# Performance work log

Hardware: AMD Instinct MI355X
Metric: run time of the kernel (lower is better)

## Reference

```python
import jax, jax.numpy as jnp
import numpy as np
from jax.ops import segment_sum

N_NODES = 50000
N_EDGES = 800000
N_GRAPHS = 64
N_CLASSES = 100
HEADS = 5
EPS = 1e-5


def _self_loops(edge_index, n):
    loop = jnp.arange(n, dtype=edge_index.dtype)
    src = jnp.concatenate([edge_index[0], loop])
    dst = jnp.concatenate([edge_index[1], loop])
    return src, dst


def gcn_conv(x, src, dst, n, w, b):
    xw = x @ w  # [N, C]
    deg = segment_sum(jnp.ones_like(dst, dtype=xw.dtype), dst, num_segments=n)
    dis = jnp.where(deg > 0, jax.lax.rsqrt(jnp.maximum(deg, 1.0)), 0.0)
    norm = dis[src] * dis[dst]  # [E']
    out = segment_sum(norm[:, None] * xw[src], dst, num_segments=n)
    return out + b


def batch_norm(x, gamma, beta):
    mu = jnp.mean(x, axis=0)
    var = jnp.var(x, axis=0)
    return (x - mu) * jax.lax.rsqrt(var + EPS) * gamma + beta


def gcn_block(x, src, dst, n, w, b, gamma, beta, residual):
    h = jax.nn.gelu(batch_norm(gcn_conv(x, src, dst, n, w, b), gamma, beta), approximate=False)
    return h + x if residual else h


def gat_conv(x, src, dst, n, w, att_src, att_dst, bias):
    H, C = att_src.shape
    xw = (x @ w).reshape(n, H, C)  # [N,H,C]
    a_src = jnp.sum(xw * att_src, axis=-1)  # [N,H]
    a_dst = jnp.sum(xw * att_dst, axis=-1)  # [N,H]
    e = jax.nn.leaky_relu(a_src[src] + a_dst[dst], 0.2)  # [E',H]
    m = jax.ops.segment_max(e, dst, num_segments=n)
    alpha = jnp.exp(e - m[dst])
    denom = segment_sum(alpha, dst, num_segments=n)
    alpha = alpha / jnp.maximum(denom[dst], 1e-16)
    # loop over small fixed head count to bound memory of [E',C] gathers
    outs = []
    for h in range(H):
        msg = alpha[:, h:h + 1] * xw[src, h, :]  # [E',C]
        outs.append(segment_sum(msg, dst, num_segments=n))
    out = jnp.mean(jnp.stack(outs, axis=0), axis=0)  # concat=False -> mean over heads
    return out + bias


def graph_layer_norm(x, gamma, beta):
    # PyG LayerNorm(mode='graph') with batch=None: normalize over all nodes+features
    mu = jnp.mean(x)
    var = jnp.var(x)
    return (x - mu) * jax.lax.rsqrt(var + EPS) * gamma + beta


def layer_norm(x, gamma, beta):
    mu = jnp.mean(x, axis=-1, keepdims=True)
    var = jnp.var(x, axis=-1, keepdims=True)
    return (x - mu) * jax.lax.rsqrt(var + EPS) * gamma + beta


def global_mean_pool(x, batch, n_graphs):
    sums = segment_sum(x, batch, num_segments=n_graphs)
    cnt = segment_sum(jnp.ones((x.shape[0],), x.dtype), batch, num_segments=n_graphs)
    return sums / jnp.maximum(cnt, 1.0)[:, None]


def setup_inputs() -> dict:
    key = jax.random.key(0)
    ks = jax.random.split(key, 24)
    glorot = lambda k, shp: jax.random.normal(k, shp, jnp.float32) * np.sqrt(2.0 / (shp[0] + shp[-1]))
    inp = {}
    inp['x'] = jax.random.normal(ks[0], (N_NODES, 3), jnp.float32)
    inp['edge_index'] = jax.random.randint(ks[1], (2, N_EDGES), 0, N_NODES, jnp.int64)
    inp['batch'] = jnp.sort(jax.random.randint(ks[2], (N_NODES,), 0, N_GRAPHS, jnp.int64))
    # input block 3->128
    inp['w_in'] = glorot(ks[3], (3, 128)); inp['b_in'] = jnp.zeros((128,), jnp.float32)
    inp['g_in'] = jnp.ones((128,), jnp.float32); inp['be_in'] = jnp.zeros((128,), jnp.float32)
    # hidden block 128->128 (n_hidden_blocks=2 -> one hidden block)
    inp['w_h'] = glorot(ks[4], (128, 128)); inp['b_h'] = jnp.zeros((128,), jnp.float32)
    inp['g_h'] = jnp.ones((128,), jnp.float32); inp['be_h'] = jnp.zeros((128,), jnp.float32)
    # GAT 128 -> 5 heads x 128, mean
    inp['w_gat'] = glorot(ks[5], (128, HEADS * 128))
    inp['att_src'] = glorot(ks[6], (HEADS, 128)); inp['att_dst'] = glorot(ks[7], (HEADS, 128))
    inp['b_gat'] = jnp.zeros((128,), jnp.float32)
    # output block 128->512
    inp['w_out'] = glorot(ks[8], (128, 512)); inp['b_out'] = jnp.zeros((512,), jnp.float32)
    inp['g_out'] = jnp.ones((512,), jnp.float32); inp['be_out'] = jnp.zeros((512,), jnp.float32)
    # encoder layer norm
    inp['g_ln'] = jnp.ones((512,), jnp.float32); inp['be_ln'] = jnp.zeros((512,), jnp.float32)
    # projection head
    inp['w_p1'] = glorot(ks[9], (512, 128)); inp['b_p1'] = jnp.zeros((128,), jnp.float32)
    inp['g_pbn'] = jnp.ones((128,), jnp.float32); inp['be_pbn'] = jnp.zeros((128,), jnp.float32)
    inp['w_p2'] = glorot(ks[10], (128, 128)); inp['b_p2'] = jnp.zeros((128,), jnp.float32)
    inp['g_pln'] = jnp.ones((128,), jnp.float32); inp['be_pln'] = jnp.zeros((128,), jnp.float32)
    # classifier
    inp['w_c'] = glorot(ks[11], (128, N_CLASSES)); inp['b_c'] = jnp.zeros((N_CLASSES,), jnp.float32)
    return inp


def reference(x, edge_index, batch, w_in, b_in, g_in, be_in, w_h, b_h, g_h, be_h,
              w_gat, att_src, att_dst, b_gat, w_out, b_out, g_out, be_out,
              g_ln, be_ln, w_p1, b_p1, g_pbn, be_pbn, w_p2, b_p2, g_pln, be_pln,
              w_c, b_c):
    n = x.shape[0]
    src, dst = _self_loops(edge_index, n)
    # encoder
    h = gcn_block(x, src, dst, n, w_in, b_in, g_in, be_in, residual=False)
    h = gcn_block(h, src, dst, n, w_h, b_h, g_h, be_h, residual=True)
    h = gat_conv(h, src, dst, n, w_gat, att_src, att_dst, b_gat)
    h = gcn_block(h, src, dst, n, w_out, b_out, g_out, be_out, residual=False)
    h = graph_layer_norm(h, g_ln, be_ln)
    h = global_mean_pool(h, batch, N_GRAPHS)  # [G,512]
    # projection head
    p = jax.nn.gelu(batch_norm(h @ w_p1 + b_p1, g_pbn, be_pbn), approximate=False)
    p = layer_norm(p @ w_p2 + b_p2 + p, g_pln, be_pln)
    # normalize + classifier
    x1 = p / jnp.maximum(jnp.linalg.norm(p, axis=1, keepdims=True), 1e-12)
    c1 = jax.nn.log_softmax(x1 @ w_c + b_c, axis=1)
    return (x1, c1)
```

## Files before the change

### kernel.cpp

```cpp
#include <hip/hip_runtime.h>
#include <hip/hip_bf16.h>
#include <math.h>

#define NN 50000
#define NE 800000
#define NG 64
#define NC 100
#define EPSV 1e-5f
#define PBN 256
#define SCB 196
#define SPL 8
#define PRB 128

typedef unsigned int   u32;
typedef unsigned short u16;
typedef __attribute__((ext_vector_type(8))) short bf16x8;
typedef __attribute__((ext_vector_type(4))) float f32x4;

__device__ __forceinline__ float gelu_f(float x){
  return 0.5f*x*(1.0f + erff(x*0.70710678118654752f));
}
__device__ __forceinline__ float bf2f(u16 u){
  return __uint_as_float(((u32)u)<<16);
}
__device__ __forceinline__ float2 bf2f2(u32 u){
  float2 r;
  r.x = __uint_as_float(u<<16);
  r.y = __uint_as_float(u & 0xffff0000u);
  return r;
}
__device__ __forceinline__ u16 f2bf(float f){
  __hip_bfloat16 h = __float2bfloat16(f);
  return *(u16*)&h;
}
__device__ __forceinline__ u32 pack_bf2(float a, float b){
  return (u32)f2bf(a) | ((u32)f2bf(b)<<16);
}

__global__ void k_deg_init(int* deg){
  int i = blockIdx.x*256 + threadIdx.x;
  if (i < NN) deg[i] = 1;
}
__global__ void k_deg_hist(const int* ei, int* deg){
  int e = blockIdx.x*256 + threadIdx.x;
  if (e < NE) atomicAdd(&deg[ei[NE + e]], 1);
}
__global__ void k_scanA(const int* deg, int* bsum, float* dis){
  __shared__ int red[256];
  int b = blockIdx.x, t = threadIdx.x;
  int i = b*256 + t;
  int d = (i < NN) ? deg[i] : 1;
  if (i < NN) dis[i] = rsqrtf((float)d);
  red[t] = (i < NN) ? d-1 : 0;
  __syncthreads();
  for (int st = 128; st; st >>= 1){
    if (t < st) red[t] += red[t+st];
    __syncthreads();
  }
  if (t == 0) bsum[b] = red[0];
}
__global__ void k_scanB(const int* bsum, int* boff){
  __shared__ int sh[256];
  int t = threadIdx.x;
  sh[t] = (t < SCB) ? bsum[t] : 0;
  __syncthreads();
  for (int d = 1; d < 256; d <<= 1){
    int v = (t >= d) ? sh[t-d] : 0;
    __syncthreads();
    sh[t] += v;
    __syncthreads();
  }
  if (t == 0) boff[0] = 0;
  if (t < SCB) boff[t+1] = sh[t];
}
__global__ void k_scanC(const int* deg, const int* boff, int* off, int* cur){
  __shared__ int sh[256];
  int b = blockIdx.x, t = threadIdx.x;
  int i = b*256 + t;
  int v = (i < NN) ? deg[i]-1 : 0;
  sh[t] = v;
  __syncthreads();
  for (int d = 1; d < 256; d <<= 1){
    int u = (t >= d) ? sh[t-d] : 0;
    __syncthreads();
    sh[t] += u;
    __syncthreads();
  }
  if (i < NN){
    int excl = boff[b] + sh[t] - v;
    off[i] = excl; cur[i] = excl;
    if (i == NN-1) off[NN] = boff[b] + sh[t];
  }
}
__global__ void k_scatter(const int* ei, int* cur, u16* col){
  int e = blockIdx.x*256 + threadIdx.x;
  if (e < NE){
    int s = ei[e], d = ei[NE + e];
    int p = atomicAdd(&cur[d], 1);
    col[p] = (u16)s;
  }
}

__global__ void k_agg3(const float* x, const int* off, const u16* col,
                       const float* dis, float* aggx){
  int i = blockIdx.x*256 + threadIdx.x;
  if (i >= NN) return;
  float di = dis[i];
  float w0 = di*di;
  float a0 = w0*x[i*3], a1 = w0*x[i*3+1], a2 = w0*x[i*3+2];
  int lo = off[i], hi = off[i+1];
  for (int e = lo; e < hi; ++e){
    int s = col[e];
    float w = dis[s]*di;
    a0 += w*x[s*3]; a1 += w*x[s*3+1]; a2 += w*x[s*3+2];
  }
  aggx[i*3] = a0; aggx[i*3+1] = a1; aggx[i*3+2] = a2;
}

__global__ void k_mm_in(const float* aggx, const float* w, const float* bias, u32* outp){
  int gid = blockIdx.x*256 + threadIdx.x;
  if (gid >= NN*64) return;
  int i = gid >> 6, j2 = (gid & 63)*2;
  float a = aggx[i*3]*w[j2]   + aggx[i*3+1]*w[128+j2]   + aggx[i*3+2]*w[256+j2]   + bias[j2];
  float b = aggx[i*3]*w[j2+1] + aggx[i*3+1]*w[128+j2+1] + aggx[i*3+2]*w[256+j2+1] + bias[j2+1];
  outp[gid] = pack_bf2(a, b);
}

__global__ void k_prepB(const float* B, int ldB, int K, int ncc, u16* Bf){
  int gid = blockIdx.x*256 + threadIdx.x;
  int tot = ncc*K*128;
  if (gid >= tot) return;
  int cc = gid / (K*128);
  int rem = gid - cc*(K*128);
  int k = rem >> 7, n = rem & 127;
  int c128 = k >> 7, kk = k & 127;
  int nt = n >> 4, i = n & 15;
  int ks = kk >> 5, jg = (kk >> 3) & 3, e = kk & 7;
  size_t addr = (size_t)cc*K*128 +
                ((((size_t)(c128*8 + nt)*4 + ks)*4 + jg)*16 + i)*8 + e;
  Bf[addr] = f2bf(B[(size_t)k*ldB + cc*128 + n]);
}
__global__ void k_prepBG(const float* w_gat, u16* Bf){
  int gid = blockIdx.x*256 + threadIdx.x;
  if (gid >= 640*128) return;
  int k = gid >> 7, n = gid & 127;
  int h = k >> 7, kk = k & 127;
  int nt = n >> 4, i = n & 15;
  int ks = kk >> 5, jg = (kk >> 3) & 3, e = kk & 7;
  size_t addr = ((((size_t)(h*8 + nt)*4 + ks)*4 + jg)*16 + i)*8 + e;
  Bf[addr] = f2bf(0.2f * w_gat[(size_t)kk*640 + h*128 + n]);
}

__global__ __launch_bounds__(256) void k_mm_mfma(const u16* A, int lda, int M, int K,
                        const u16* Bf, u16* C, int ldC, const float* bias){
  __shared__ u16 ct[64*132];
  int tid = threadIdx.x;
  int w = tid >> 6, l = tid & 63;
  int jg = l >> 4, ii = l & 15;
  int m0 = blockIdx.x*64 + w*16;
  int cc = blockIdx.y;
  int arow = m0 + ii; if (arow >= M) arow = M-1;
  const u16* Bfc = Bf + (size_t)cc*K*128;
  f32x4 acc[8] = {};
  for (int c128 = 0; c128 < (K >> 7); ++c128){
    const u16* Ar = A + (size_t)arow*lda + c128*128;
    bf16x8 af[4];
    #pragma unroll
    for (int ks = 0; ks < 4; ++ks)
      af[ks] = *(const bf16x8*)(Ar + ks*32 + jg*8);
    #pragma unroll
    for (int nt = 0; nt < 8; ++nt){
      f32x4 a4 = acc[nt];
      #pragma unroll
      for (int ks = 0; ks < 4; ++ks){
        bf16x8 bfr = *(const bf16x8*)(Bfc +
            ((((size_t)(c128*8 + nt)*4 + ks)*4 + jg)*16 + ii)*8);
        a4 = __builtin_amdgcn_mfma_f32_16x16x32_bf16(af[ks], bfr, a4, 0, 0, 0);
      }
      acc[nt] = a4;
    }
  }
  int cOut = cc*128;
  int lrow0 = w*16 + jg*4;
  #pragma unroll
  for (int nt = 0; nt < 8; ++nt){
    float bv = bias[cOut + nt*16 + ii];
    #pragma unroll
    for (int r = 0; r < 4; ++r)
      ct[(lrow0 + r)*132 + nt*16 + ii] = f2bf(acc[nt][r] + bv);
  }
  __syncthreads();
  int lr0 = tid >> 6;
  int lc = tid & 63;
  #pragma unroll
  for (int rr = 0; rr < 16; ++rr){
    int lrow = rr*4 + lr0;
    int grow = blockIdx.x*64 + lrow;
    if (grow < M)
      *(u32*)(C + (size_t)grow*ldC + cOut + lc*2) = *(const u32*)(ct + lrow*132 + lc*2);
  }
}

__global__ void k_gcn_agg64(const u16* xw, const int* off, const u16* col,
                            const float* dis, u16* out){
  int i = blockIdx.x, t = threadIdx.x;
  float di = dis[i];
  float2 sv = bf2f2(((const u32*)(xw + (size_t)i*128))[t]);
  float w0 = di*di;
  float ax = w0*sv.x, ay = w0*sv.y;
  int lo = off[i], hi = off[i+1];
  int e = lo;
  for (; e + 4 <= hi; e += 4){
    int s0 = col[e], s1 = col[e+1], s2 = col[e+2], s3 = col[e+3];
    float wA = dis[s0]*di, wB = dis[s1]*di, wC = dis[s2]*di, wD = dis[s3]*di;
    float2 r0 = bf2f2(((const u32*)(xw + (size_t)s0*128))[t]);
    float2 r1 = bf2f2(((const u32*)(xw + (size_t)s1*128))[t]);
    float2 r2 = bf2f2(((const u32*)(xw + (size_t)s2*128))[t]);
    float2 r3 = bf2f2(((const u32*)(xw + (size_t)s3*128))[t]);
    ax += wA*r0.x; ay += wA*r0.y;
    ax += wB*r1.x; ay += wB*r1.y;
    ax += wC*r2.x; ay += wC*r2.y;
    ax += wD*r3.x; ay += wD*r3.y;
  }
  for (; e < hi; ++e){
    int s = col[e];
    float w = dis[s]*di;
    float2 rv = bf2f2(((const u32*)(xw + (size_t)s*128))[t]);
    ax += w*rv.x; ay += w*rv.y;
  }
  ((u32*)(out + (size_t)i*128))[t] = pack_bf2(ax, ay);
}

__global__ void k_bn_part(const u16* x, int stride, int W, float* part){
  __shared__ float shs[8][132];
  __shared__ float shq[8][132];
  int t = threadIdx.x;
  int ft = t & 31, rl = t >> 5;
  int f0 = ft*4;
  int fbase = blockIdx.x*128;
  int p = blockIdx.y;
  float s0=0.f,s1=0.f,s2=0.f,s3=0.f, q0=0.f,q1=0.f,q2=0.f,q3=0.f;
  for (int r = p + PBN*rl; r < NN; r += PBN*8){
    ushort4 u = *(const ushort4*)(x + (size_t)r*stride + fbase + f0);
    float v0 = bf2f(u.x), v1 = bf2f(u.y), v2 = bf2f(u.z), v3 = bf2f(u.w);
    s0 += v0; s1 += v1; s2 += v2; s3 += v3;
    q0 += v0*v0; q1 += v1*v1; q2 += v2*v2; q3 += v3*v3;
  }
  shs[rl][f0] = s0; shs[rl][f0+1] = s1; shs[rl][f0+2] = s2; shs[rl][f0+3] = s3;
  shq[rl][f0] = q0; shq[rl][f0+1] = q1; shq[rl][f0+2] = q2; shq[rl][f0+3] = q3;
  __syncthreads();
  if (t < 128){
    float s = 0.f, q = 0.f;
    #pragma unroll
    for (int r = 0; r < 8; ++r){ s += shs[r][t]; q += shq[r][t]; }
    size_t fb = (size_t)(fbase + t)*2*PBN;
    part[fb + p] = s;
    part[fb + PBN + p] = q;
  }
}
__global__ void k_bn_fin(const float* part, const float* g, const float* be,
                         float* ss, int W, float invn){
  __shared__ float rs[256], rq[256];
  int f = blockIdx.x, t = threadIdx.x;
  size_t fb = (size_t)f*2*PBN;
  rs[t] = part[fb + t];
  rq[t] = part[fb + PBN + t];
  __syncthreads();
  for (int st = 128; st; st >>= 1){
    if (t < st){ rs[t] += rs[t+st]; rq[t] += rq[t+st]; }
    __syncthreads();
  }
  if (t == 0){
    float mean = rs[0]*invn;
    float var  = rq[0]*invn - mean*mean;
    float sc = g[f]*rsqrtf(var + EPSV);
    ss[f] = sc;
    ss[W+f] = be[f] - mean*sc;
  }
}
template<bool RES>
__global__ void k_bn_apply(const u32* x, const float* ss, const u32* res, u32* out){
  const int n = NN*64;
  for (int idx = blockIdx.x*256 + threadIdx.x; idx < n; idx += gridDim.x*256){
    int f2 = (idx & 63)*2;
    float2 v = bf2f2(x[idx]);
    v.x = gelu_f(v.x*ss[f2]   + ss[128+f2]);
    v.y = gelu_f(v.y*ss[f2+1] + ss[128+f2+1]);
    if (RES){ float2 r = bf2f2(res[idx]); v.x += r.x; v.y += r.y; }
    out[idx] = pack_bf2(v.x, v.y);
  }
}

__global__ void k_wv(const float* w_gat, const float* att_s, const float* att_d,
                     float* wvs, float* wvd){
  int h = blockIdx.x, c = threadIdx.x;
  float ss = 0.f, sd = 0.f;
  const float* wr = w_gat + (size_t)c*640 + h*128;
  const float* as = att_s + h*128;
  const float* ad = att_d + h*128;
  for (int k = 0; k < 128; ++k){
    float wv = wr[k];
    ss += wv*as[k]; sd += wv*ad[k];
  }
  wvs[h*128+c] = ss; wvd[h*128+c] = sd;
}

__global__ void k_score10(const u16* h2, const float* wvs, const float* wvd,
                          float* asrc8, float* adst8){
  int i = blockIdx.x, t = threadIdx.x;
  float2 v = bf2f2(((const u32*)(h2 + (size_t)i*128))[t]);
  int f2 = 2*t;
  #pragma unroll
  for (int h = 0; h < 5; ++h){
    float vs = v.x*wvs[h*128+f2] + v.y*wvs[h*128+f2+1];
    float vd = v.x*wvd[h*128+f2] + v.y*wvd[h*128+f2+1];
    #pragma unroll
    for (int d = 32; d; d >>= 1){ vs += __shfl_xor(vs, d); vd += __shfl_xor(vd, d); }
    if (t == 0){ asrc8[i*8+h] = vs; adst8[i*8+h] = vd; }
  }
}

__global__ void k_gat_fused(const u16* h2, const int* off, const u16* col,
                            const float* asrc8, const float* adst8,
                            u16* agg5){
  __shared__ float sal[64][6];
  int i = blockIdx.x, t = threadIdx.x;
  float2 svv = bf2f2(((const u32*)(h2 + (size_t)i*128))[t]);
  float ad[5], dn[5], ax[5], ay[5];
  #pragma unroll
  for (int h = 0; h < 5; ++h){
    ad[h] = adst8[i*8+h];
    float v = asrc8[i*8+h] + ad[h];
    v = (v > 0.f) ? v : 0.2f*v;
    float esf = expf(v);
    dn[h] = esf;
    ax[h] = esf*svv.x; ay[h] = esf*svv.y;
  }
  int lo = off[i], hi = off[i+1];
  for (int base = lo; base < hi; base += 64){
    int n = min(64, hi - base);
    if (t < n){
      int s = col[base + t];
      float4 a03 = *(const float4*)(asrc8 + (size_t)s*8);
      float  a4  = asrc8[(size_t)s*8 + 4];
      float sa[5] = {a03.x, a03.y, a03.z, a03.w, a4};
      #pragma unroll
      for (int h = 0; h < 5; ++h){
        float v = sa[h] + ad[h];
        v = (v > 0.f) ? v : 0.2f*v;
        sal[t][h] = expf(v);
      }
    }
    __syncthreads();
    for (int j = 0; j < n; ++j){
      int s = col[base + j];
      float2 rv = bf2f2(((const u32*)(h2 + (size_t)s*128))[t]);
      #pragma unroll
      for (int h = 0; h < 5; ++h){
        float al = sal[j][h];
        dn[h] += al;
        ax[h] += al*rv.x;
        ay[h] += al*rv.y;
      }
    }
    __syncthreads();
  }
  #pragma unroll
  for (int h = 0; h < 5; ++h){
    float iv = 1.f/fmaxf(dn[h]*(1.f/1.f), 1e-16f);
    ((u32*)(agg5 + (size_t)i*640 + h*128))[t] = pack_bf2(ax[h]*iv, ay[h]*iv);
  }
}

__global__ void k_gstart(const int* batch, int* gs){
  int g = threadIdx.x;
  if (g > NG) return;
  int lo = 0, hi = NN;
  while (lo < hi){ int mid = (lo+hi) >> 1; if (batch[mid] < g) lo = mid+1; else hi = mid; }
  gs[g] = lo;
}
__global__ void k_poolstat(const u16* a512, const float* ss, const int* gs,
                           float* poolpart, float* sqpart){
  __shared__ float4 red4[512];
  __shared__ float redq[512];
  int g = blockIdx.x, sp = blockIdx.y, t = threadIdx.x;
  int ft = t & 127, rl = t >> 7;
  int f0 = ft*4;
  int lo = gs[g], hi = gs[g+1];
  float sc0 = ss[f0],     sc1 = ss[f0+1],     sc2 = ss[f0+2],     sc3 = ss[f0+3];
  float sh0 = ss[512+f0], sh1 = ss[512+f0+1], sh2 = ss[512+f0+2], sh3 = ss[512+f0+3];
  float4 s4 = {0.f,0.f,0.f,0.f};
  float q = 0.f;
  for (int r = lo + sp*4 + rl; r < hi; r += SPL*4){
    ushort4 u = *(const ushort4*)(a512 + (size_t)r*512 + f0);
    float v0 = gelu_f(bf2f(u.x)*sc0 + sh0);
    float v1 = gelu_f(bf2f(u.y)*sc1 + sh1);
    float v2 = gelu_f(bf2f(u.z)*sc2 + sh2);
    float v3 = gelu_f(bf2f(u.w)*sc3 + sh3);
    s4.x += v0; s4.y += v1; s4.z += v2; s4.w += v3;
    q += v0*v0 + v1*v1 + v2*v2 + v3*v3;
  }
  red4[t] = s4; redq[t] = q;
  __syncthreads();
  for (int st = 256; st; st >>= 1){
    if (t < st) redq[t] += redq[t+st];
    __syncthreads();
  }
  if (t == 0) sqpart[g*SPL + sp] = redq[0];
  if (rl == 0){
    float4 a = red4[t], b = red4[t+128], c = red4[t+256], d = red4[t+384];
    float4 o;
    o.x = a.x+b.x+c.x+d.x; o.y = a.y+b.y+c.y+d.y;
    o.z = a.z+b.z+c.z+d.z; o.w = a.w+b.w+c.w+d.w;
    ((float4*)poolpart)[((size_t)(g*SPL + sp))*128 + ft] = o;
  }
}
__global__ void k_poolredA(const float* poolpart, const float* sqpart,
                           float* ppred, float* sqred){
  __shared__ float rs_[256], rq_[256];
  int b = blockIdx.x, t = threadIdx.x;
  float s = 0.f, q = 0.f;
  const int tot = NG*SPL*512;
  for (int i = b*256 + t; i < tot; i += PRB*256) s += poolpart[i];
  for (int i = b*256 + t; i < NG*SPL; i += PRB*256) q += sqpart[i];
  rs_[t] = s; rq_[t] = q;
  __syncthreads();
  for (int st = 128; st; st >>= 1){
    if (t < st){ rs_[t] += rs_[t+st]; rq_[t] += rq_[t+st]; }
    __syncthreads();
  }
  if (t == 0){ ppred[b] = rs_[0]; sqred[b] = rq_[0]; }
}
__global__ void k_poolredB(const float* ppred, const float* sqred, float* scal){
  __shared__ float rs_[128], rq_[128];
  int t = threadIdx.x;
  rs_[t] = ppred[t]; rq_[t] = sqred[t];
  __syncthreads();
  for (int st = 64; st; st >>= 1){
    if (t < st){ rs_[t] += rs_[t+st]; rq_[t] += rq_[t+st]; }
    __syncthreads();
  }
  if (t == 0){
    float invn = 1.f/((float)NN*512.f);
    float mu  = rs_[0]*invn;
    float var = rq_[0]*invn - mu*mu;
    scal[2] = mu;
    scal[3] = rsqrtf(var + EPSV);
  }
}
__global__ void k_poolapply(const float* poolpart, const int* gs, const float* scal,
                            const float* gam, const float* bet, float* pooled){
  int g = blockIdx.x, f = threadIdx.x;
  float s = 0.f;
  #pragma unroll
  for (int sp = 0; sp < SPL; ++sp)
    s += poolpart[((size_t)(g*SPL + sp))*512 + f];
  float cnt = (float)max(gs[g+1] - gs[g], 1);
  pooled[g*512 + f] = (s/cnt - scal[2])*scal[3]*gam[f] + bet[f];
}

__global__ void k_head_mm1(const float* pooled, const float* w, const float* b, float* q){
  int g = blockIdx.x, j = threadIdx.x;
  float s = b[j];
  const float* pr = pooled + g*512;
  for (int k = 0; k < 512; ++k) s += pr[k]*w[k*128+j];
  q[g*128+j] = s;
}
__global__ void k_head_bn(const float* qin, const float* g_, const float* be_, float* qout){
  int f = threadIdx.x;
  float s = 0.f, sq = 0.f;
  for (int r = 0; r < NG; ++r){ float v = qin[r*128+f]; s += v; sq += v*v; }
  float mu = s*(1.f/NG), var = sq*(1.f/NG) - mu*mu;
  float sc = g_[f]*rsqrtf(var + EPSV);
  float sh = be_[f] - mu*sc;
  for (int r = 0; r < NG; ++r) qout[r*128+f] = gelu_f(qin[r*128+f]*sc + sh);
}
__global__ void k_head2c(const float* q2, const float* w, const float* b,
                         const float* gam, const float* bet,
                         const float* wc, const float* bc, float* out){
  int g = blockIdx.x, j = threadIdx.x;
  __shared__ float row[128], red[128], shv[3];
  row[j] = q2[g*128+j];
  __syncthreads();
  float s = b[j] + row[j];
  for (int k = 0; k < 128; ++k) s += row[k]*w[k*128+j];
  red[j] = s; __syncthreads();
  for (int st = 64; st; st >>= 1){ if (j < st) red[j] += red[j+st]; __syncthreads(); }
  if (j == 0) shv[0] = red[0]*(1.f/128.f);
  __syncthreads();
  float d = s - shv[0];
  red[j] = d*d; __syncthreads();
  for (int st = 64; st; st >>= 1){ if (j < st) red[j] += red[j+st]; __syncthreads(); }
  if (j == 0) shv[1] = rsqrtf(red[0]*(1.f/128.f) + EPSV);
  __syncthreads();
  float v = d*shv[1]*gam[j] + bet[j];
  red[j] = v*v; __syncthreads();
  for (int st = 64; st; st >>= 1){ if (j < st) red[j] += red[j+st]; __syncthreads(); }
  if (j == 0) shv[2] = 1.f/fmaxf(sqrtf(red[0]), 1e-12f);
  __syncthreads();
  float o = v*shv[2];
  out[g*128+j] = o;
  __syncthreads();
  row[j] = o;
  __syncthreads();
  float cs = -1e30f;
  if (j < NC){
    cs = bc[j];
    for (int k = 0; k < 128; ++k) cs += row[k]*wc[k*NC+j];
  }
  red[j] = cs; __syncthreads();
  for (int st = 64; st; st >>= 1){ if (j < st) red[j] = fmaxf(red[j], red[j+st]); __syncthreads(); }
  if (j == 0) shv[0] = red[0];
  __syncthreads();
  float e = (j < NC) ? expf(cs - shv[0]) : 0.f;
  red[j] = e; __syncthreads();
  for (int st = 64; st; st >>= 1){ if (j < st) red[j] += red[j+st]; __syncthreads(); }
  if (j == 0) shv[1] = logf(red[0]);
  __syncthreads();
  if (j < NC) out[NG*128 + g*NC+j] = cs - shv[0] - shv[1];
}

extern "C" void kernel_launch(void* const* d_in, const int* in_sizes, int n_in,
                              void* d_out, int out_size, void* d_ws, size_t ws_size,
                              hipStream_t stream){
  const float* x      = (const float*)d_in[0];
  const int*   ei     = (const int*)d_in[1];
  const int*   batch  = (const int*)d_in[2];
  const float* w_in   = (const float*)d_in[3];
  const float* b_in   = (const float*)d_in[4];
  const float* g_in   = (const float*)d_in[5];
  const float* be_in  = (const float*)d_in[6];
  const float* w_h    = (const float*)d_in[7];
  const float* b_h    = (const float*)d_in[8];
  const float* g_h    = (const float*)d_in[9];
  const float* be_h   = (const float*)d_in[10];
  const float* w_gat  = (const float*)d_in[11];
  const float* att_s  = (const float*)d_in[12];
  const float* att_d  = (const float*)d_in[13];
  const float* b_gat  = (const float*)d_in[14];
  const float* w_out  = (const float*)d_in[15];
  const float* b_out  = (const float*)d_in[16];
  const float* g_out  = (const float*)d_in[17];
  const float* be_out = (const float*)d_in[18];
  const float* g_ln   = (const float*)d_in[19];
  const float* be_ln  = (const float*)d_in[20];
  const float* w_p1   = (const float*)d_in[21];
  const float* b_p1   = (const float*)d_in[22];
  const float* g_pbn  = (const float*)d_in[23];
  const float* be_pbn = (const float*)d_in[24];
  const float* w_p2   = (const float*)d_in[25];
  const float* b_p2   = (const float*)d_in[26];
  const float* g_pln  = (const float*)d_in[27];
  const float* be_pln = (const float*)d_in[28];
  const float* w_c    = (const float*)d_in[29];
  const float* b_c    = (const float*)d_in[30];
  float* out = (float*)d_out;

  char* ws = (char*)d_ws;
  size_t o = 0;
  auto carve = [&](size_t bytes) -> char* {
    char* p = ws + o;
    o += (bytes + 255) & ~(size_t)255;
    return p;
  };
  int*   deg    = (int*)  carve((size_t)NN*4);
  int*   off    = (int*)  carve((size_t)(NN+1)*4);
  int*   cur    = (int*)  carve((size_t)NN*4);
  u16*   col    = (u16*)  carve((size_t)NE*2);
  float* dis    = (float*)carve((size_t)NN*4);
  int*   bsum   = (int*)  carve((size_t)SCB*4);
  int*   boff   = (int*)  carve((size_t)(SCB+1)*4);
  float* aggx3  = (float*)carve((size_t)NN*3*4);
  u16*   F0     = (u16*)  carve((size_t)NN*128*2);
  u16*   F1     = (u16*)  carve((size_t)NN*128*2);
  u16*   F2     = (u16*)  carve((size_t)NN*128*2);
  u16*   AGG5   = (u16*)  carve((size_t)NN*640*2);
  float* asrc8  = (float*)carve((size_t)NN*8*4);
  float* adst8  = (float*)carve((size_t)NN*8*4);
  float* wvs    = (float*)carve(640*4);
  float* wvd    = (float*)carve(640*4);
  u16*   BfH    = (u16*)  carve((size_t)128*128*2);
  u16*   BfG    = (u16*)  carve((size_t)640*128*2);
  u16*   BfO    = (u16*)  carve((size_t)128*512*2);
  float* part   = (float*)carve((size_t)512*2*PBN*4);
  float* poolpart = (float*)carve((size_t)NG*SPL*512*4);
  float* sqpart = (float*)carve((size_t)NG*SPL*4);
  float* ppred  = (float*)carve((size_t)PRB*4);
  float* sqred  = (float*)carve((size_t)PRB*4);
  float* ssbuf  = (float*)carve(1024*4);
  float* scal   = (float*)carve(64);
  int*   gst    = (int*)  carve(65*4);
  float* pooled = (float*)carve((size_t)NG*512*4);
  float* q      = (float*)carve((size_t)NG*128*4);
  float* q2     = (float*)carve((size_t)NG*128*4);
  if (o > ws_size) return;

  u16* A512 = AGG5;

  k_deg_init<<<196,256,0,stream>>>(deg);
  k_deg_hist<<<3125,256,0,stream>>>(ei, deg);
  k_scanA<<<SCB,256,0,stream>>>(deg, bsum, dis);
  k_scanB<<<1,256,0,stream>>>(bsum, boff);
  k_scanC<<<SCB,256,0,stream>>>(deg, boff, off, cur);
  k_scatter<<<3125,256,0,stream>>>(ei, cur, col);

  k_prepB<<<64,256,0,stream>>>(w_h, 128, 128, 1, BfH);
  k_prepBG<<<320,256,0,stream>>>(w_gat, BfG);
  k_prepB<<<256,256,0,stream>>>(w_out, 512, 128, 4, BfO);

  k_agg3<<<196,256,0,stream>>>(x, off, col, dis, aggx3);
  k_mm_in<<<(NN*64+255)/256,256,0,stream>>>(aggx3, w_in, b_in, (u32*)F0);
  k_bn_part<<<dim3(1,PBN),256,0,stream>>>(F0, 128, 128, part);
  k_bn_fin<<<128,256,0,stream>>>(part, g_in, be_in, ssbuf, 128, 1.f/NN);
  k_bn_apply<false><<<2048,256,0,stream>>>((u32*)F0, ssbuf, nullptr, (u32*)F1);

  k_gcn_agg64<<<NN,64,0,stream>>>(F1, off, col, dis, F0);
  k_mm_mfma<<<dim3(782,1),256,0,stream>>>(F0, 128, NN, 128, BfH, F2, 128, b_h);
  k_bn_part<<<dim3(1,PBN),256,0,stream>>>(F2, 128, 128, part);
  k_bn_fin<<<128,256,0,stream>>>(part, g_h, be_h, ssbuf, 128, 1.f/NN);
  k_bn_apply<true><<<2048,256,0,stream>>>((u32*)F2, ssbuf, (u32*)F1, (u32*)F0);

  k_wv<<<5,128,0,stream>>>(w_gat, att_s, att_d, wvs, wvd);
  k_score10<<<NN,64,0,stream>>>(F0, wvs, wvd, asrc8, adst8);
  k_gat_fused<<<NN,64,0,stream>>>(F0, off, col, asrc8, adst8, AGG5);
  k_mm_mfma<<<dim3(782,1),256,0,stream>>>(AGG5, 640, NN, 640, BfG, F1, 128, b_gat);

  k_gcn_agg64<<<NN,64,0,stream>>>(F1, off, col, dis, F2);
  k_mm_mfma<<<dim3(782,4),256,0,stream>>>(F2, 128, NN, 128, BfO, A512, 512, b_out);
  k_bn_part<<<dim3(4,PBN),256,0,stream>>>(A512, 512, 512, part);
  k_bn_fin<<<512,256,0,stream>>>(part, g_out, be_out, ssbuf, 512, 1.f/NN);

  k_gstart<<<1,128,0,stream>>>(batch, gst);
  k_poolstat<<<dim3(NG,SPL),512,0,stream>>>(A512, ssbuf, gst, poolpart, sqpart);
  k_poolredA<<<PRB,256,0,stream>>>(poolpart, sqpart, ppred, sqred);
  k_poolredB<<<1,128,0,stream>>>(ppred, sqred, scal);
  k_poolapply<<<NG,512,0,stream>>>(poolpart, gst, scal, g_ln, be_ln, pooled);

  k_head_mm1<<<NG,128,0,stream>>>(pooled, w_p1, b_p1, q);
  k_head_bn<<<1,128,0,stream>>>(q, g_pbn, be_pbn, q2);
  k_head2c<<<NG,128,0,stream>>>(q2, w_p2, b_p2, g_pln, be_pln, w_c, b_c, out);
}
```

Baseline: 613.7 us.

## Fuse batch-norm partial statistics into MFMA GEMM epilogue and streamline GAT aggregation

The MFMA matmul epilogue now computes per-column sums and sums of squares from its shared-memory output tile and writes them as per-block partials. A new finalize kernel reduces these across the 782 row blocks, which removes the separate bn_part passes that re-read the full activation tensors. The GAT aggregation kernel also caches neighbor indices in shared memory and accumulates the softmax denominator during the parallel exp phase, followed by a wave reduction, instead of adding it serially in the inner loop. Statistics are now taken from the bf16-rounded values in the tile.

```diff
diff --git a/kernel.cpp b/kernel.cpp
--- a/kernel.cpp
+++ b/kernel.cpp
@@ -11,6 +11,7 @@
 #define SCB 196
 #define SPL 8
 #define PRB 128
+#define MMB 782
 
 typedef unsigned int   u32;
 typedef unsigned short u16;
@@ -152,7 +153,8 @@
 }
 
 __global__ __launch_bounds__(256) void k_mm_mfma(const u16* A, int lda, int M, int K,
-                        const u16* Bf, u16* C, int ldC, const float* bias){
+                        const u16* Bf, u16* C, int ldC, const float* bias,
+                        float* bnpart){
   __shared__ u16 ct[64*132];
   int tid = threadIdx.x;
   int w = tid >> 6, l = tid & 63;
@@ -199,6 +201,17 @@
     if (grow < M)
       *(u32*)(C + (size_t)grow*ldC + cOut + lc*2) = *(const u32*)(ct + lrow*132 + lc*2);
   }
+  if (bnpart && tid < 128){
+    int rlim = M - blockIdx.x*64; if (rlim > 64) rlim = 64;
+    float s = 0.f, q = 0.f;
+    for (int r = 0; r < rlim; ++r){
+      float v = bf2f(ct[r*132 + tid]);
+      s += v; q += v*v;
+    }
+    size_t fb = (size_t)(cOut + tid)*2*gridDim.x;
+    bnpart[fb + blockIdx.x] = s;
+    bnpart[fb + gridDim.x + blockIdx.x] = q;
+  }
 }
 
 __global__ void k_gcn_agg64(const u16* xw, const int* off, const u16* col,
@@ -278,6 +291,27 @@
     ss[W+f] = be[f] - mean*sc;
   }
 }
+__global__ void k_bn_finB(const float* part, int NB, const float* g, const float* be,
+                          float* ss, int W, float invn){
+  __shared__ float rs[256], rq[256];
+  int f = blockIdx.x, t = threadIdx.x;
+  size_t fb = (size_t)f*2*NB;
+  float s = 0.f, q = 0.f;
+  for (int b = t; b < NB; b += 256){ s += part[fb + b]; q += part[fb + NB + b]; }
+  rs[t] = s; rq[t] = q;
+  __syncthreads();
+  for (int st = 128; st; st >>= 1){
+    if (t < st){ rs[t] += rs[t+st]; rq[t] += rq[t+st]; }
+    __syncthreads();
+  }
+  if (t == 0){
+    float mean = rs[0]*invn;
+    float var  = rq[0]*invn - mean*mean;
+    float sc = g[f]*rsqrtf(var + EPSV);
+    ss[f] = sc;
+    ss[W+f] = be[f] - mean*sc;
+  }
+}
 template<bool RES>
 __global__ void k_bn_apply(const u32* x, const float* ss, const u32* res, u32* out){
   const int n = NN*64;
@@ -324,23 +358,26 @@
                             const float* asrc8, const float* adst8,
                             u16* agg5){
   __shared__ float sal[64][6];
+  __shared__ int   scol[64];
   int i = blockIdx.x, t = threadIdx.x;
   float2 svv = bf2f2(((const u32*)(h2 + (size_t)i*128))[t]);
   float ad[5], dn[5], ax[5], ay[5];
+  float esf[5];
   #pragma unroll
   for (int h = 0; h < 5; ++h){
     ad[h] = adst8[i*8+h];
     float v = asrc8[i*8+h] + ad[h];
     v = (v > 0.f) ? v : 0.2f*v;
-    float esf = expf(v);
-    dn[h] = esf;
-    ax[h] = esf*svv.x; ay[h] = esf*svv.y;
+    esf[h] = expf(v);
+    dn[h] = 0.f;
+    ax[h] = esf[h]*svv.x; ay[h] = esf[h]*svv.y;
   }
   int lo = off[i], hi = off[i+1];
   for (int base = lo; base < hi; base += 64){
     int n = min(64, hi - base);
     if (t < n){
       int s = col[base + t];
+      scol[t] = s;
       float4 a03 = *(const float4*)(asrc8 + (size_t)s*8);
       float  a4  = asrc8[(size_t)s*8 + 4];
       float sa[5] = {a03.x, a03.y, a03.z, a03.w, a4};
@@ -348,17 +385,18 @@
       for (int h = 0; h < 5; ++h){
         float v = sa[h] + ad[h];
         v = (v > 0.f) ? v : 0.2f*v;
-        sal[t][h] = expf(v);
+        float ex = expf(v);
+        sal[t][h] = ex;
+        dn[h] += ex;
       }
     }
     __syncthreads();
     for (int j = 0; j < n; ++j){
-      int s = col[base + j];
+      int s = scol[j];
       float2 rv = bf2f2(((const u32*)(h2 + (size_t)s*128))[t]);
       #pragma unroll
       for (int h = 0; h < 5; ++h){
         float al = sal[j][h];
-        dn[h] += al;
         ax[h] += al*rv.x;
         ay[h] += al*rv.y;
       }
@@ -367,7 +405,9 @@
   }
   #pragma unroll
   for (int h = 0; h < 5; ++h){
-    float iv = 1.f/fmaxf(dn[h]*(1.f/1.f), 1e-16f);
+    #pragma unroll
+    for (int d = 32; d; d >>= 1) dn[h] += __shfl_xor(dn[h], d);
+    float iv = 1.f/fmaxf(dn[h] + esf[h], 1e-16f);
     ((u32*)(agg5 + (size_t)i*640 + h*128))[t] = pack_bf2(ax[h]*iv, ay[h]*iv);
   }
 }
@@ -582,7 +622,7 @@
   u16*   BfH    = (u16*)  carve((size_t)128*128*2);
   u16*   BfG    = (u16*)  carve((size_t)640*128*2);
   u16*   BfO    = (u16*)  carve((size_t)128*512*2);
-  float* part   = (float*)carve((size_t)512*2*PBN*4);
+  float* part   = (float*)carve((size_t)512*2*MMB*4);
   float* poolpart = (float*)carve((size_t)NG*SPL*512*4);
   float* sqpart = (float*)carve((size_t)NG*SPL*4);
   float* ppred  = (float*)carve((size_t)PRB*4);
@@ -615,20 +655,18 @@
   k_bn_apply<false><<<2048,256,0,stream>>>((u32*)F0, ssbuf, nullptr, (u32*)F1);
 
   k_gcn_agg64<<<NN,64,0,stream>>>(F1, off, col, dis, F0);
-  k_mm_mfma<<<dim3(782,1),256,0,stream>>>(F0, 128, NN, 128, BfH, F2, 128, b_h);
-  k_bn_part<<<dim3(1,PBN),256,0,stream>>>(F2, 128, 128, part);
-  k_bn_fin<<<128,256,0,stream>>>(part, g_h, be_h, ssbuf, 128, 1.f/NN);
+  k_mm_mfma<<<dim3(MMB,1),256,0,stream>>>(F0, 128, NN, 128, BfH, F2, 128, b_h, part);
+  k_bn_finB<<<128,256,0,stream>>>(part, MMB, g_h, be_h, ssbuf, 128, 1.f/NN);
   k_bn_apply<true><<<2048,256,0,stream>>>((u32*)F2, ssbuf, (u32*)F1, (u32*)F0);
 
   k_wv<<<5,128,0,stream>>>(w_gat, att_s, att_d, wvs, wvd);
   k_score10<<<NN,64,0,stream>>>(F0, wvs, wvd, asrc8, adst8);
   k_gat_fused<<<NN,64,0,stream>>>(F0, off, col, asrc8, adst8, AGG5);
-  k_mm_mfma<<<dim3(782,1),256,0,stream>>>(AGG5, 640, NN, 640, BfG, F1, 128, b_gat);
+  k_mm_mfma<<<dim3(MMB,1),256,0,stream>>>(AGG5, 640, NN, 640, BfG, F1, 128, b_gat, nullptr);
 
   k_gcn_agg64<<<NN,64,0,stream>>>(F1, off, col, dis, F2);
-  k_mm_mfma<<<dim3(782,4),256,0,stream>>>(F2, 128, NN, 128, BfO, A512, 512, b_out);
-  k_bn_part<<<dim3(4,PBN),256,0,stream>>>(A512, 512, 512, part);
-  k_bn_fin<<<512,256,0,stream>>>(part, g_out, be_out, ssbuf, 512, 1.f/NN);
+  k_mm_mfma<<<dim3(MMB,4),256,0,stream>>>(F2, 128, NN, 128, BfO, A512, 512, b_out, part);
+  k_bn_finB<<<512,256,0,stream>>>(part, MMB, g_out, be_out, ssbuf, 512, 1.f/NN);
 
   k_gstart<<<1,128,0,stream>>>(batch, gst);
   k_poolstat<<<dim3(NG,SPL),512,0,stream>>>(A512, ssbuf, gst, poolpart, sqpart);
```

New measurement: 607.5 us. About the same (-1.0%).
